# Optimization experiments

Hardware: AMD Instinct MI355X
Metric: run time of the kernel (lower is better)

Reference implementation:

```python
import jax, jax.numpy as jnp
import numpy as np

EPS = 1e-6
N_NFT, N_TRADER, D = 16384, 8192, 8
NNZ = 2_000_000


def setup_inputs() -> dict:
    key = jax.random.key(0)
    k1, k2, k3, k4, k5, k6, k7 = jax.random.split(key, 7)
    return {
        "latent_z": jax.random.normal(k1, (N_NFT, D), dtype=jnp.float32),
        "latent_q": jax.random.normal(k2, (N_TRADER, D), dtype=jnp.float32),
        "gamma": jax.random.normal(k3, (N_NFT,), dtype=jnp.float32),
        "delta": jax.random.normal(k4, (N_TRADER,), dtype=jnp.float32),
        "weights": jax.random.uniform(k5, (NNZ,), dtype=jnp.float32),
        "sparse_i": jax.random.randint(k6, (NNZ,), 0, N_NFT, dtype=jnp.int64) if jax.config.jax_enable_x64 else jax.random.randint(k6, (NNZ,), 0, N_NFT, dtype=jnp.int32),
        "sparse_j": jax.random.randint(k7, (NNZ,), 0, N_TRADER, dtype=jnp.int32),
    }


def reference(latent_z, latent_q, gamma, delta, weights, sparse_i, sparse_j):
    # --- dense normalizer: exp(gamma)^T @ exp(-(cdist(z+eps, q)+eps)) @ exp(delta)
    z = latent_z + EPS  # torch.cdist(self.latent_z + 1e-6, self.latent_q)
    zn = jnp.sum(z * z, axis=-1)                     # [N]
    qn = jnp.sum(latent_q * latent_q, axis=-1)       # [M]
    d2 = zn[:, None] + qn[None, :] - 2.0 * (z @ latent_q.T)  # [N, M]
    dist = jnp.sqrt(jnp.maximum(d2, 0.0))
    mat = jnp.exp(-(dist + EPS))                     # [N, M]
    z_pdist1 = jnp.exp(gamma) @ mat @ jnp.exp(delta)  # scalar

    # --- sparse Poisson log-likelihood term over observed edges
    diff = latent_z[sparse_i] - latent_q[sparse_j] + EPS  # [nnz, D]
    zqdist = -jnp.sqrt(jnp.sum(diff * diff, axis=-1))     # [nnz]
    z_pdist2 = jnp.sum(weights * (gamma[sparse_i] + delta[sparse_j] + zqdist))

    return z_pdist2 - z_pdist1
```

## Files before the change

kernel.cpp:

```cpp
#include <hip/hip_runtime.h>

#define EPSF 1e-6f
#define L2E  1.44269504088896340736f

using bf16x8 = __attribute__((ext_vector_type(8))) short;
using f32x16 = __attribute__((ext_vector_type(16))) float;

constexpr int NT   = 256;
constexpr int JC   = 512;
constexpr int NJC  = 8192 / JC;
constexpr int RPAN = 128;
constexpr int NRP  = 16384 / RPAN;
constexpr int NB   = NRP * NJC;
constexpr int JT   = JC / 32;

__device__ __forceinline__ short f2bf(float f) {
    union { float f; unsigned u; } c{f};
    return (short)((c.u + 0x7fffu + ((c.u >> 16) & 1u)) >> 16);
}
__device__ __forceinline__ float bf2f(short s) {
    union { unsigned u; float f; } c{((unsigned)(unsigned short)s) << 16};
    return c.f;
}

__device__ __forceinline__ float block_reduce_sum(float v) {
#pragma unroll
    for (int off = 32; off > 0; off >>= 1) v += __shfl_down(v, off, 64);
    __shared__ float parts[4];
    const int t = threadIdx.x;
    if ((t & 63) == 0) parts[t >> 6] = v;
    __syncthreads();
    float r = 0.f;
    if (t == 0) r = parts[0] + parts[1] + parts[2] + parts[3];
    return r;
}

__device__ __forceinline__ bf16x8 make_afrag(const float* __restrict__ z,
                                             int row, int half) {
    const float4 a = *(const float4*)(z + (size_t)row * 8);
    const float4 b = *(const float4*)(z + (size_t)row * 8 + 4);
    const float h[8] = {L2E * (a.x + EPSF), L2E * (a.y + EPSF),
                        L2E * (a.z + EPSF), L2E * (a.w + EPSF),
                        L2E * (b.x + EPSF), L2E * (b.y + EPSF),
                        L2E * (b.z + EPSF), L2E * (b.w + EPSF)};
    short s[8];
    float zn = 0.f;
#pragma unroll
    for (int d = 0; d < 8; ++d) {
        s[d] = f2bf(h[d]);
        const float r = bf2f(s[d]);
        zn = fmaf(r, r, zn);
    }
    bf16x8 f;
    if (half == 0) {
        f[0] = s[0]; f[1] = s[1]; f[2] = s[2]; f[3] = s[3];
        f[4] = s[4]; f[5] = s[5]; f[6] = s[6]; f[7] = s[7];
    } else {
        f[0] = f2bf(zn); f[1] = (short)0x3F80;
        f[2] = 0; f[3] = 0; f[4] = 0; f[5] = 0; f[6] = 0; f[7] = 0;
    }
    return f;
}

__global__ __launch_bounds__(NT) void fused_kernel(
    const float* __restrict__ z, const float* __restrict__ q,
    const float* __restrict__ gamma, const float* __restrict__ delta,
    const float* __restrict__ w, const int* __restrict__ si,
    const int* __restrict__ sj, int nnz, float* __restrict__ partial)
{
    __shared__ __align__(16) short sqb[1024 * 8];
    __shared__ float sld[JC];
    __shared__ float seg[RPAN];

    const int t    = threadIdx.x;
    const int id   = blockIdx.x;
    const int jc   = id & (NJC - 1);
    const int rpan = id >> 4;
    const int c0   = jc * JC;
    const int r0   = rpan * RPAN;

    if (t < RPAN) seg[t] = __expf(gamma[r0 + t]);

#pragma unroll
    for (int c = t; c < JC; c += NT) {
        const int C = c0 + c;
        const float4 a = *(const float4*)(q + (size_t)C * 8);
        const float4 b = *(const float4*)(q + (size_t)C * 8 + 4);
        const float h[8] = {L2E * a.x, L2E * a.y, L2E * a.z, L2E * a.w,
                            L2E * b.x, L2E * b.y, L2E * b.z, L2E * b.w};
        bf16x8 g0;
        float qn = 0.f;
#pragma unroll
        for (int d = 0; d < 8; ++d) {
            const short s = f2bf(h[d]);
            const float r = bf2f(s);
            qn = fmaf(r, r, qn);
            g0[d] = f2bf(-2.f * r);
        }
        *(bf16x8*)&sqb[c * 8] = g0;
        bf16x8 g1;
        g1[0] = (short)0x3F80;
        g1[1] = f2bf(qn);
        g1[2] = 0; g1[3] = 0; g1[4] = 0; g1[5] = 0; g1[6] = 0; g1[7] = 0;
        *(bf16x8*)&sqb[(512 + c) * 8] = g1;
        sld[c] = L2E * (delta[C] - EPSF);
    }

    const int wv   = t >> 6;
    const int lane = t & 63;
    const int li   = lane & 31;
    const int half = lane >> 5;
    const bf16x8 afrag = make_afrag(z, r0 + wv * 32 + li, half);

    float sacc = 0.f;
    for (int k = id * NT + t; k < nnz; k += NB * NT) {
        const int i = si[k];
        const int j = sj[k];
        const float4 a = *(const float4*)(z + (size_t)i * 8);
        const float4 b = *(const float4*)(z + (size_t)i * 8 + 4);
        const float4 c = *(const float4*)(q + (size_t)j * 8);
        const float4 d = *(const float4*)(q + (size_t)j * 8 + 4);
        const float d0 = a.x - c.x + EPSF, d1 = a.y - c.y + EPSF;
        const float d2 = a.z - c.z + EPSF, d3 = a.w - c.w + EPSF;
        const float d4 = b.x - d.x + EPSF, d5 = b.y - d.y + EPSF;
        const float d6 = b.z - d.z + EPSF, d7 = b.w - d.w + EPSF;
        float s2 = d0 * d0;
        s2 = fmaf(d1, d1, s2); s2 = fmaf(d2, d2, s2); s2 = fmaf(d3, d3, s2);
        s2 = fmaf(d4, d4, s2); s2 = fmaf(d5, d5, s2); s2 = fmaf(d6, d6, s2);
        s2 = fmaf(d7, d7, s2);
        sacc = fmaf(w[k], gamma[i] + delta[j] - __builtin_amdgcn_sqrtf(s2), sacc);
    }
    __syncthreads();

    const short* bbase = &sqb[(half * 512 + li) * 8];

    float acc[16];
#pragma unroll
    for (int r = 0; r < 16; ++r) acc[r] = 0.f;

#pragma unroll
    for (int jt = 0; jt < JT; ++jt) {
        const bf16x8 bfrag = *(const bf16x8*)(bbase + jt * 32 * 8);
        const float  ld_l  = sld[jt * 32 + li];
        f32x16 s = __builtin_amdgcn_mfma_f32_32x32x16_bf16(
            afrag, bfrag, (f32x16)(0.f), 0, 0, 0);
#pragma unroll
        for (int r = 0; r < 16; ++r) {
            const float st = __builtin_amdgcn_sqrtf(__builtin_fabsf(s[r]));
            acc[r] += __builtin_amdgcn_exp2f(ld_l - st);
        }
    }

    float vv = 0.f;
#pragma unroll
    for (int r4 = 0; r4 < 4; ++r4)
#pragma unroll
        for (int rr = 0; rr < 4; ++rr)
            vv = fmaf(seg[wv * 32 + half * 4 + rr + 8 * r4], acc[r4 * 4 + rr], vv);

    const float v = block_reduce_sum(sacc - vv);
    if (t == 0) partial[id] = v;
}

__global__ __launch_bounds__(256) void reduce_kernel(
    const float* __restrict__ partial, int n, float* __restrict__ out)
{
    float v = 0.f;
    for (int k = threadIdx.x; k < n; k += 256) v += partial[k];
    v = block_reduce_sum(v);
    if (threadIdx.x == 0) out[0] = v;
}

extern "C" void kernel_launch(void* const* d_in, const int* in_sizes, int n_in,
                              void* d_out, int out_size, void* d_ws, size_t ws_size,
                              hipStream_t stream) {
    const float* z     = (const float*)d_in[0];
    const float* q     = (const float*)d_in[1];
    const float* gamma = (const float*)d_in[2];
    const float* delta = (const float*)d_in[3];
    const float* w     = (const float*)d_in[4];
    const int*   si    = (const int*)d_in[5];
    const int*   sj    = (const int*)d_in[6];
    const int    nnz   = in_sizes[4];

    float* out = (float*)d_out;
    float* ws  = (float*)d_ws;

    fused_kernel<<<NB, NT, 0, stream>>>(z, q, gamma, delta, w, si, sj, nnz, ws);
    reduce_kernel<<<1, 256, 0, stream>>>(ws, NB, out);
}
```

Baseline: 49.41 us.

## Stagger sparse gather before or after dense MFMA phase by block parity

Moves the sparse edge loop into a helper and runs it either before or after the dense MFMA/exp phase, chosen by a bit of the block id. The aim is that co-resident blocks mix memory-bound gather work with ALU-bound dense work instead of all hitting memory at once. It also stores exp(delta) in shared memory and multiplies it in with an fma, replacing the subtract inside exp2. That change costs an extra multiply per element and slightly alters rounding.

New measurement: 73.91 us. +49.6%, slower.

```diff
diff --git a/kernel.cpp b/kernel.cpp
--- a/kernel.cpp
+++ b/kernel.cpp
@@ -62,58 +62,14 @@
     return f;
 }
 
-__global__ __launch_bounds__(NT) void fused_kernel(
+__device__ __forceinline__ float sparse_slice(
     const float* __restrict__ z, const float* __restrict__ q,
     const float* __restrict__ gamma, const float* __restrict__ delta,
     const float* __restrict__ w, const int* __restrict__ si,
-    const int* __restrict__ sj, int nnz, float* __restrict__ partial)
+    const int* __restrict__ sj, int nnz, int k0)
 {
-    __shared__ __align__(16) short sqb[1024 * 8];
-    __shared__ float sld[JC];
-    __shared__ float seg[RPAN];
-
-    const int t    = threadIdx.x;
-    const int id   = blockIdx.x;
-    const int jc   = id & (NJC - 1);
-    const int rpan = id >> 4;
-    const int c0   = jc * JC;
-    const int r0   = rpan * RPAN;
-
-    if (t < RPAN) seg[t] = __expf(gamma[r0 + t]);
-
-#pragma unroll
-    for (int c = t; c < JC; c += NT) {
-        const int C = c0 + c;
-        const float4 a = *(const float4*)(q + (size_t)C * 8);
-        const float4 b = *(const float4*)(q + (size_t)C * 8 + 4);
-        const float h[8] = {L2E * a.x, L2E * a.y, L2E * a.z, L2E * a.w,
-                            L2E * b.x, L2E * b.y, L2E * b.z, L2E * b.w};
-        bf16x8 g0;
-        float qn = 0.f;
-#pragma unroll
-        for (int d = 0; d < 8; ++d) {
-            const short s = f2bf(h[d]);
-            const float r = bf2f(s);
-            qn = fmaf(r, r, qn);
-            g0[d] = f2bf(-2.f * r);
-        }
-        *(bf16x8*)&sqb[c * 8] = g0;
-        bf16x8 g1;
-        g1[0] = (short)0x3F80;
-        g1[1] = f2bf(qn);
-        g1[2] = 0; g1[3] = 0; g1[4] = 0; g1[5] = 0; g1[6] = 0; g1[7] = 0;
-        *(bf16x8*)&sqb[(512 + c) * 8] = g1;
-        sld[c] = L2E * (delta[C] - EPSF);
-    }
-
-    const int wv   = t >> 6;
-    const int lane = t & 63;
-    const int li   = lane & 31;
-    const int half = lane >> 5;
-    const bf16x8 afrag = make_afrag(z, r0 + wv * 32 + li, half);
-
     float sacc = 0.f;
-    for (int k = id * NT + t; k < nnz; k += NB * NT) {
+    for (int k = k0; k < nnz; k += NB * NT) {
         const int i = si[k];
         const int j = sj[k];
         const float4 a = *(const float4*)(z + (size_t)i * 8);
@@ -130,9 +86,70 @@
         s2 = fmaf(d7, d7, s2);
         sacc = fmaf(w[k], gamma[i] + delta[j] - __builtin_amdgcn_sqrtf(s2), sacc);
     }
+    return sacc;
+}
+
+__global__ __launch_bounds__(NT) void fused_kernel(
+    const float* __restrict__ z, const float* __restrict__ q,
+    const float* __restrict__ gamma, const float* __restrict__ delta,
+    const float* __restrict__ w, const int* __restrict__ si,
+    const int* __restrict__ sj, int nnz, float* __restrict__ partial)
+{
+    __shared__ __align__(16) short sqb[1024 * 8];
+    __shared__ float sed[JC];
+    __shared__ float seg[RPAN];
+
+    const int t    = threadIdx.x;
+    const int id   = blockIdx.x;
+    const int jc   = id & (NJC - 1);
+    const int rpan = id >> 4;
+    const int c0   = jc * JC;
+    const int r0   = rpan * RPAN;
+
+    if (t < RPAN) seg[t] = __expf(gamma[r0 + t]);
+
+#pragma unroll
+    for (int c = t; c < JC; c += NT) {
+        const int C = c0 + c;
+        const float4 a = *(const float4*)(q + (size_t)C * 8);
+        const float4 b = *(const float4*)(q + (size_t)C * 8 + 4);
+        const float h[8] = {L2E * a.x, L2E * a.y, L2E * a.z, L2E * a.w,
+                            L2E * b.x, L2E * b.y, L2E * b.z, L2E * b.w};
+        bf16x8 g0;
+        float qn = 0.f;
+#pragma unroll
+        for (int d = 0; d < 8; ++d) {
+            const short s = f2bf(h[d]);
+            const float r = bf2f(s);
+            qn = fmaf(r, r, qn);
+            g0[d] = f2bf(-2.f * r);
+        }
+        *(bf16x8*)&sqb[c * 8] = g0;
+        bf16x8 g1;
+        g1[0] = (short)0x3F80;
+        g1[1] = f2bf(qn);
+        g1[2] = 0; g1[3] = 0; g1[4] = 0; g1[5] = 0; g1[6] = 0; g1[7] = 0;
+        *(bf16x8*)&sqb[(512 + c) * 8] = g1;
+        sed[c] = __expf(delta[C] - EPSF);
+    }
+
+    const int wv   = t >> 6;
+    const int lane = t & 63;
+    const int li   = lane & 31;
+    const int half = lane >> 5;
+    const bf16x8 afrag = make_afrag(z, r0 + wv * 32 + li, half);
+
+    const int  k0     = id * NT + t;
+    const bool sparse_first = ((id >> 8) & 1) == 0;
+
+    float sacc = 0.f;
+    if (sparse_first) {
+        sacc = sparse_slice(z, q, gamma, delta, w, si, sj, nnz, k0);
+    }
     __syncthreads();
 
     const short* bbase = &sqb[(half * 512 + li) * 8];
+    const float* edp   = &sed[li];
 
     float acc[16];
 #pragma unroll
@@ -141,13 +158,13 @@
 #pragma unroll
     for (int jt = 0; jt < JT; ++jt) {
         const bf16x8 bfrag = *(const bf16x8*)(bbase + jt * 32 * 8);
-        const float  ld_l  = sld[jt * 32 + li];
+        const float  ed_l  = edp[jt * 32];
         f32x16 s = __builtin_amdgcn_mfma_f32_32x32x16_bf16(
             afrag, bfrag, (f32x16)(0.f), 0, 0, 0);
 #pragma unroll
         for (int r = 0; r < 16; ++r) {
             const float st = __builtin_amdgcn_sqrtf(__builtin_fabsf(s[r]));
-            acc[r] += __builtin_amdgcn_exp2f(ld_l - st);
+            acc[r] = fmaf(ed_l, __builtin_amdgcn_exp2f(-st), acc[r]);
         }
     }
 
@@ -157,6 +174,12 @@
 #pragma unroll
         for (int rr = 0; rr < 4; ++rr)
             vv = fmaf(seg[wv * 32 + half * 4 + rr + 8 * r4], acc[r4 * 4 + rr], vv);
+
+    if (!sparse_first) {
+        __builtin_amdgcn_sched_barrier(0);
+        asm volatile("" ::: "memory");
+        sacc = sparse_slice(z, q, gamma, delta, w, si, sj, nnz, k0);
+    }
 
     const float v = block_reduce_sum(sacc - vv);
     if (t == 0) partial[id] = v;
```
